# Kernel tuning notes

Measured on AMD Instinct MI355X. Metric: run time of the kernel, lower is better.

## Reference

```python
import jax, jax.numpy as jnp
import numpy as np

N_X, N_U, N_Y = 256, 32, 32
BATCH, T = 16, 8192
LAM_MIN, LAM_MAX = 0.9, 0.995
B_SCALE, D_SCALE = 0.25, 0.25


def setup_inputs() -> dict:
    key = jax.random.key(0)
    k = jax.random.split(key, 6)
    # Orthogonal Q via QR of a random Gaussian matrix (as in the torch module)
    M = jax.random.normal(k[0], (N_X, N_X), dtype=jnp.float32)
    Q, _ = jnp.linalg.qr(M)
    lam = LAM_MIN + (LAM_MAX - LAM_MIN) * jax.random.uniform(k[1], (N_X,), dtype=jnp.float32)
    Bmat = B_SCALE * jax.random.normal(k[2], (N_X, N_U), dtype=jnp.float32)
    # C picks out the first n_y coordinates (C[i, i] = 1)
    C = jnp.eye(N_Y, N_X, dtype=jnp.float32)
    D = D_SCALE * jax.random.normal(k[3], (N_Y, N_U), dtype=jnp.float32)
    x0 = jax.random.normal(k[4], (BATCH, N_X), dtype=jnp.float32)
    u = jax.random.normal(k[5], (BATCH, T, N_U), dtype=jnp.float32)
    return {"x0": x0, "u": u, "Q": Q, "lam": lam, "Bmat": Bmat, "C": C, "D": D}


def _diag_scan(lam, v):
    """Diagonal linear recurrence x_t = lam * x_{t-1} + v_t (x_0 folded into v[:, 0]).

    lam: (N,), v: (B, T, N) -> states x_1..x_T of shape (B, T, N).
    """
    a = jnp.broadcast_to(lam, v.shape)

    def op(l, r):
        a1, b1 = l
        a2, b2 = r
        return a1 * a2, a2 * b1 + b2

    return jax.lax.associative_scan(op, (a, v), axis=1)[1]


def reference(x0, u, Q, lam, Bmat, C, D):
    Bz = Q.T @ Bmat            # (n_x, n_u) modal input matrix
    Cz = C @ Q                 # (n_y, n_x) modal output matrix
    z0 = x0 @ Q                # (B, n_x)   modal initial state
    v = jnp.einsum('btu,nu->btn', u, Bz)   # (B, T, n_x)
    v = v.at[:, 0].add(lam * z0)            # fold lam * z0 into first step
    z_next = _diag_scan(lam, v)             # (B, T, n_x) = z_1..z_T
    # y_t uses z_t for t = 0..T-1 (states[:, :-1] in the original)
    z_prev = jnp.concatenate([z0[:, None, :], z_next[:, :-1]], axis=1)
    y = jnp.einsum('btn,yn->bty', z_prev, Cz) + jnp.einsum('btu,yu->bty', u, D)
    return y
```

## Files before the change

kernel.cpp:

```cpp
#include <hip/hip_runtime.h>

typedef _Float16 half4_t __attribute__((ext_vector_type(4)));
typedef _Float16 half8_t __attribute__((ext_vector_type(8)));
typedef float f32x4 __attribute__((ext_vector_type(4)));

constexpr int NX = 256, NU = 32, NY = 32, BATCH = 16, T = 8192;
constexpr int NC = 64, L = 128;
constexpr int SUBT = 32, NSUB = L / SUBT;
constexpr int KW = NX + NU;
constexpr int VP = 40;
constexpr int ZP = 264;
constexpr int POOLSZ = NX * VP;

__global__ __launch_bounds__(256) void k_pre(
    const float* __restrict__ x0, const float* __restrict__ Q,
    const float* __restrict__ Bm, const float* __restrict__ C,
    const float* __restrict__ D,
    _Float16* __restrict__ Bzh, _Float16* __restrict__ Wh, float* __restrict__ z0)
{
    int o = blockIdx.x * 64 + (threadIdx.x >> 2);
    int p = threadIdx.x & 3;
    if (o >= 20480) {
        if (p == 0) {
            int g = o - 20480, iy = g >> 5, j = g & 31;
            Wh[iy * KW + NX + j] = (_Float16)D[iy * NU + j];
        }
        return;
    }
    float s = 0.f;
    int k0 = p * 64;
    if (o < 8192) {
        int n = o >> 5, j = o & 31;
        for (int k = k0; k < k0 + 64; ++k) s = fmaf(Q[k * NX + n], Bm[k * NU + j], s);
    } else if (o < 16384) {
        int g = o - 8192; int iy = g >> 8, nn = g & 255;
        for (int k = k0; k < k0 + 64; ++k) s = fmaf(C[iy * NX + k], Q[k * NX + nn], s);
    } else {
        int g = o - 16384; int b = g >> 8, nn = g & 255;
        for (int k = k0; k < k0 + 64; ++k) s = fmaf(x0[b * NX + k], Q[k * NX + nn], s);
    }
    s += __shfl_xor(s, 1);
    s += __shfl_xor(s, 2);
    if (p == 0) {
        if (o < 8192) {
            Bzh[o] = (_Float16)s;
        } else if (o < 16384) {
            int g = o - 8192; int iy = g >> 8, nn = g & 255;
            Wh[iy * KW + nn] = (_Float16)s;
        } else {
            z0[o - 16384] = s;
        }
    }
}

__global__ __launch_bounds__(256) void k_phase1(
    const float* __restrict__ u, const float* __restrict__ lam,
    const _Float16* __restrict__ Bzh, float* __restrict__ S)
{
    __shared__ __align__(16) _Float16 ut[2][SUBT][32];

    const int b = blockIdx.x >> 6, c = blockIdx.x & 63, tid = threadIdx.x;
    const int w = tid >> 6, lane = tid & 63, m16 = lane & 15, quad = lane >> 4;

    half8_t bfrag[4];
    #pragma unroll
    for (int i = 0; i < 4; ++i)
        bfrag[i] = *(const half8_t*)&Bzh[((4 * w + i) * 16 + m16) * NU + quad * 8];

    float wr[4][4], wt16[4], l32[4], acc[4];
    #pragma unroll
    for (int i = 0; i < 4; ++i) {
        float la = lam[(4 * w + i) * 16 + m16];
        float p2 = la * la, p4 = p2 * p2, p8 = p4 * p4, p16 = p8 * p8;
        float inv1 = 1.0f / la;
        float inv4 = (inv1 * inv1) * (inv1 * inv1);
        float pq = 1.0f;
        if (quad & 1) pq *= inv4;
        if (quad & 2) pq *= inv4 * inv4;
        float w0 = (p16 * p8 * p4 * p2 * la) * pq;
        wr[i][0] = w0;
        wr[i][1] = w0 * inv1;
        wr[i][2] = wr[i][1] * inv1;
        wr[i][3] = wr[i][2] * inv1;
        wt16[i] = 1.0f / p16;
        l32[i] = p16 * p16;
        acc[i] = 0.f;
    }

    const float* ug = u + ((size_t)(b * T) + (size_t)c * L) * NU;

    for (int sub = 0; sub < NSUB; ++sub) {
        {
            float4 uu = *(const float4*)(ug + (size_t)sub * SUBT * NU + tid * 4);
            int tr = tid >> 3, cb = ((tid & 7) * 4 + (tr & 3) * 8) & 31;
            half4_t h; h.x = (_Float16)uu.x; h.y = (_Float16)uu.y;
            h.z = (_Float16)uu.z; h.w = (_Float16)uu.w;
            *(half4_t*)&ut[sub & 1][tr][cb] = h;
        }
        __syncthreads();
        int rot = (m16 & 3) * 8;
        half8_t af0 = *(const half8_t*)&ut[sub & 1][m16][(quad * 8 + rot) & 31];
        half8_t af1 = *(const half8_t*)&ut[sub & 1][16 + m16][(quad * 8 + rot) & 31];
        #pragma unroll
        for (int i = 0; i < 4; ++i) {
            f32x4 z4 = {0.f, 0.f, 0.f, 0.f};
            f32x4 v0 = __builtin_amdgcn_mfma_f32_16x16x32_f16(af0, bfrag[i], z4, 0, 0, 0);
            f32x4 v1 = __builtin_amdgcn_mfma_f32_16x16x32_f16(af1, bfrag[i], z4, 0, 0, 0);
            float s0 = wr[i][0] * v0[0] + wr[i][1] * v0[1] + wr[i][2] * v0[2] + wr[i][3] * v0[3];
            float s1 = wr[i][0] * v1[0] + wr[i][1] * v1[1] + wr[i][2] * v1[2] + wr[i][3] * v1[3];
            acc[i] = fmaf(l32[i], acc[i], fmaf(wt16[i], s1, s0));
        }
    }
    #pragma unroll
    for (int i = 0; i < 4; ++i) {
        acc[i] += __shfl_xor(acc[i], 16);
        acc[i] += __shfl_xor(acc[i], 32);
    }
    float out = quad == 0 ? acc[0] : quad == 1 ? acc[1] : quad == 2 ? acc[2] : acc[3];
    S[(size_t)blockIdx.x * NX + (4 * w + quad) * 16 + m16] = out;
}

__global__ __launch_bounds__(256) void k_phase2(
    const float* __restrict__ z0, const float* __restrict__ lam,
    const float* __restrict__ S, float* __restrict__ P)
{
    int b = blockIdx.x, n = threadIdx.x;
    float ln = lam[n], lamL = ln;
    #pragma unroll
    for (int i = 0; i < 7; ++i) lamL *= lamL;
    float cur = z0[b * NX + n];
    P[(size_t)(b * NC) * NX + n] = cur;
    for (int c = 1; c < NC; ++c) {
        cur = fmaf(lamL, cur, S[(size_t)(b * NC + c - 1) * NX + n]);
        P[(size_t)(b * NC + c) * NX + n] = cur;
    }
}

__global__ __launch_bounds__(256) void k_phase3(
    const float* __restrict__ u, const float* __restrict__ lam,
    const _Float16* __restrict__ Bzh, const _Float16* __restrict__ Wh,
    const float* __restrict__ P, float* __restrict__ y)
{
    __shared__ __align__(16) _Float16 ut[2][SUBT][32];
    __shared__ __align__(16) _Float16 pool[POOLSZ];

    const int b = blockIdx.x >> 6, c = blockIdx.x & 63, tid = threadIdx.x;
    const int w = tid >> 6, lane = tid & 63, m16 = lane & 15, quad = lane >> 4;
    const int tw = w & 1, yw = w >> 1;

    half8_t bfrag[4];
    #pragma unroll
    for (int i = 0; i < 4; ++i)
        bfrag[i] = *(const half8_t*)&Bzh[((4 * w + i) * 16 + m16) * NU + quad * 8];
    half8_t wfrag[9];
    #pragma unroll
    for (int kk = 0; kk < 9; ++kk)
        wfrag[kk] = *(const half8_t*)&Wh[(yw * 16 + m16) * KW + kk * 32 + quad * 8];
    half8_t triA[2];
    #pragma unroll
    for (int tt = 0; tt < 2; ++tt) {
        #pragma unroll
        for (int j = 0; j < 8; ++j)
            triA[tt][j] = (_Float16)((quad * 8 + j < tt * 16 + m16) ? 1.f : 0.f);
    }

    float lamn[4], inv1[4], iq[4], i16p[4], fq[4], f16p[4], l32[4], p[4];
    #pragma unroll
    for (int i = 0; i < 4; ++i) {
        int ni = (4 * w + i) * 16 + m16;
        float la = lam[ni];
        lamn[i] = la;
        float p2 = la * la, p4 = p2 * p2, p8 = p4 * p4, p16 = p8 * p8;
        float iv = 1.0f / la;
        inv1[i] = iv;
        float iv4 = (iv * iv) * (iv * iv);
        float pqi = 1.0f, pqf = 1.0f;
        if (quad & 1) { pqi *= iv4; pqf *= p4; }
        if (quad & 2) { pqi *= iv4 * iv4; pqf *= p8; }
        iq[i] = iv * pqi;
        fq[i] = pqf;
        i16p[i] = 1.0f / p16;
        f16p[i] = p16;
        l32[i] = p16 * p16;
        p[i] = P[(size_t)(b * NC + c) * NX + ni];
    }

    const float* ug = u + ((size_t)(b * T) + (size_t)c * L) * NU;
    float* yg = y + ((size_t)(b * T) + (size_t)c * L) * NY;

    for (int sub = 0; sub < NSUB; ++sub) {
        {
            float4 uu = *(const float4*)(ug + (size_t)sub * SUBT * NU + tid * 4);
            int tr = tid >> 3, cb = ((tid & 7) * 4 + (tr & 3) * 8) & 31;
            half4_t h; h.x = (_Float16)uu.x; h.y = (_Float16)uu.y;
            h.z = (_Float16)uu.z; h.w = (_Float16)uu.w;
            *(half4_t*)&ut[sub & 1][tr][cb] = h;
        }
        __syncthreads();

        int rot = (m16 & 3) * 8;
        half8_t af0 = *(const half8_t*)&ut[sub & 1][m16][(quad * 8 + rot) & 31];
        half8_t af1 = *(const half8_t*)&ut[sub & 1][16 + m16][(quad * 8 + rot) & 31];
        float partial[4];
        #pragma unroll
        for (int i = 0; i < 4; ++i) {
            int ni = (4 * w + i) * 16 + m16;
            f32x4 z4 = {0.f, 0.f, 0.f, 0.f};
            f32x4 v0 = __builtin_amdgcn_mfma_f32_16x16x32_f16(af0, bfrag[i], z4, 0, 0, 0);
            f32x4 v1 = __builtin_amdgcn_mfma_f32_16x16x32_f16(af1, bfrag[i], z4, 0, 0, 0);
            float ps = 0.f;
            float sc = iq[i];
            half4_t h0, h1;
            #pragma unroll
            for (int r = 0; r < 4; ++r) {
                float a0 = v0[r] * sc;
                float a1 = v1[r] * (sc * i16p[i]);
                ps += a0 + a1;
                h0[r] = (_Float16)a0;
                h1[r] = (_Float16)a1;
                sc *= inv1[i];
            }
            partial[i] = ps;
            *(half4_t*)&pool[ni * VP + quad * 4] = h0;
            *(half4_t*)&pool[ni * VP + 16 + quad * 4] = h1;
        }
        __syncthreads();

        f32x4 zp0[4], zp1[4];
        #pragma unroll
        for (int i = 0; i < 4; ++i) {
            int ni = (4 * w + i) * 16 + m16;
            half8_t bV = *(const half8_t*)&pool[ni * VP + quad * 8];
            f32x4 z4 = {0.f, 0.f, 0.f, 0.f};
            zp0[i] = __builtin_amdgcn_mfma_f32_16x16x32_f16(triA[0], bV, z4, 0, 0, 0);
            zp1[i] = __builtin_amdgcn_mfma_f32_16x16x32_f16(triA[1], bV, z4, 0, 0, 0);
        }
        __syncthreads();

        #pragma unroll
        for (int i = 0; i < 4; ++i) {
            int ni = (4 * w + i) * 16 + m16;
            float f = fq[i];
            #pragma unroll
            for (int r = 0; r < 4; ++r) {
                float zv0 = f * (p[i] + zp0[i][r]);
                float zv1 = (f * f16p[i]) * (p[i] + zp1[i][r]);
                pool[(quad * 4 + r) * ZP + ni] = (_Float16)zv0;
                pool[(16 + quad * 4 + r) * ZP + ni] = (_Float16)zv1;
                f *= lamn[i];
            }
        }
        #pragma unroll
        for (int i = 0; i < 4; ++i) {
            float ps = partial[i];
            ps += __shfl_xor(ps, 16);
            ps += __shfl_xor(ps, 32);
            p[i] = l32[i] * (p[i] + ps);
        }
        __syncthreads();

        f32x4 acc = {0.f, 0.f, 0.f, 0.f};
        #pragma unroll
        for (int kk = 0; kk < 8; ++kk) {
            half8_t az = *(const half8_t*)&pool[(tw * 16 + m16) * ZP + kk * 32 + quad * 8];
            acc = __builtin_amdgcn_mfma_f32_16x16x32_f16(az, wfrag[kk], acc, 0, 0, 0);
        }
        {
            half8_t au = *(const half8_t*)&ut[sub & 1][tw * 16 + m16][(quad * 8 + rot) & 31];
            acc = __builtin_amdgcn_mfma_f32_16x16x32_f16(au, wfrag[8], acc, 0, 0, 0);
        }
        #pragma unroll
        for (int r = 0; r < 4; ++r)
            yg[(size_t)(sub * SUBT + tw * 16 + quad * 4 + r) * NY + yw * 16 + m16] = acc[r];
    }
}

extern "C" void kernel_launch(void* const* d_in, const int* in_sizes, int n_in,
                              void* d_out, int out_size, void* d_ws, size_t ws_size,
                              hipStream_t stream) {
    (void)in_sizes; (void)n_in; (void)out_size; (void)ws_size;
    const float* x0  = (const float*)d_in[0];
    const float* u   = (const float*)d_in[1];
    const float* Q   = (const float*)d_in[2];
    const float* lam = (const float*)d_in[3];
    const float* Bm  = (const float*)d_in[4];
    const float* C   = (const float*)d_in[5];
    const float* D   = (const float*)d_in[6];
    float* y = (float*)d_out;

    char* ws = (char*)d_ws;
    _Float16* Bzh = (_Float16*)(ws);
    _Float16* Wh  = (_Float16*)(ws + 16384);
    float*    z0  = (float*)(ws + 34816);
    float*    S   = (float*)(ws + 51200);
    float*    P   = (float*)(ws + 51200 + 1048576);

    k_pre   <<<336, 256, 0, stream>>>(x0, Q, Bm, C, D, Bzh, Wh, z0);
    k_phase1<<<BATCH * NC, 256, 0, stream>>>(u, lam, Bzh, S);
    k_phase2<<<BATCH, 256, 0, stream>>>(z0, lam, S, P);
    k_phase3<<<BATCH * NC, 256, 0, stream>>>(u, lam, Bzh, Wh, P, y);
}
```

Baseline: 119.8 us.

## Fold chunk-prefix carry computation into phase3, removing the phase2 kernel

Drops the serial per-batch phase2 kernel that scanned chunk summaries into carry-in states. Each phase3 block now recomputes its own carry-in by summing all earlier chunk summaries, weighted by powers of lam^L, plus the decayed z0, and stages the result in shared memory. This removes one kernel launch and a long serial 64-step dependency chain that ran on only 16 blocks. In exchange, the carry work becomes redundant and quadratic in chunk count, up to 63 loads per thread in late chunks, and a block-wide barrier is added.

```diff
diff --git a/kernel.cpp b/kernel.cpp
--- a/kernel.cpp
+++ b/kernel.cpp
@@ -120,33 +120,32 @@
     S[(size_t)blockIdx.x * NX + (4 * w + quad) * 16 + m16] = out;
 }
 
-__global__ __launch_bounds__(256) void k_phase2(
-    const float* __restrict__ z0, const float* __restrict__ lam,
-    const float* __restrict__ S, float* __restrict__ P)
-{
-    int b = blockIdx.x, n = threadIdx.x;
-    float ln = lam[n], lamL = ln;
-    #pragma unroll
-    for (int i = 0; i < 7; ++i) lamL *= lamL;
-    float cur = z0[b * NX + n];
-    P[(size_t)(b * NC) * NX + n] = cur;
-    for (int c = 1; c < NC; ++c) {
-        cur = fmaf(lamL, cur, S[(size_t)(b * NC + c - 1) * NX + n]);
-        P[(size_t)(b * NC + c) * NX + n] = cur;
-    }
-}
-
 __global__ __launch_bounds__(256) void k_phase3(
     const float* __restrict__ u, const float* __restrict__ lam,
     const _Float16* __restrict__ Bzh, const _Float16* __restrict__ Wh,
-    const float* __restrict__ P, float* __restrict__ y)
+    const float* __restrict__ S, const float* __restrict__ z0,
+    float* __restrict__ y)
 {
     __shared__ __align__(16) _Float16 ut[2][SUBT][32];
     __shared__ __align__(16) _Float16 pool[POOLSZ];
+    __shared__ float pvec[NX];
 
     const int b = blockIdx.x >> 6, c = blockIdx.x & 63, tid = threadIdx.x;
     const int w = tid >> 6, lane = tid & 63, m16 = lane & 15, quad = lane >> 4;
     const int tw = w & 1, yw = w >> 1;
+
+    {
+        float la = lam[tid], lamL = la;
+        #pragma unroll
+        for (int i = 0; i < 7; ++i) lamL *= lamL;
+        const float* Sb = S + (size_t)(b * NC) * NX;
+        float pv = 0.f, wgt = 1.f;
+        for (int cc = c - 1; cc >= 0; --cc) {
+            pv = fmaf(wgt, Sb[(size_t)cc * NX + tid], pv);
+            wgt *= lamL;
+        }
+        pvec[tid] = fmaf(wgt, z0[b * NX + tid], pv);
+    }
 
     half8_t bfrag[4];
     #pragma unroll
@@ -182,11 +181,15 @@
         i16p[i] = 1.0f / p16;
         f16p[i] = p16;
         l32[i] = p16 * p16;
-        p[i] = P[(size_t)(b * NC + c) * NX + ni];
-    }
+    }
+    __syncthreads();
+    #pragma unroll
+    for (int i = 0; i < 4; ++i)
+        p[i] = pvec[(4 * w + i) * 16 + m16];
 
     const float* ug = u + ((size_t)(b * T) + (size_t)c * L) * NU;
     float* yg = y + ((size_t)(b * T) + (size_t)c * L) * NY;
+    const int rot = (m16 & 3) * 8;
 
     for (int sub = 0; sub < NSUB; ++sub) {
         {
@@ -198,7 +201,6 @@
         }
         __syncthreads();
 
-        int rot = (m16 & 3) * 8;
         half8_t af0 = *(const half8_t*)&ut[sub & 1][m16][(quad * 8 + rot) & 31];
         half8_t af1 = *(const half8_t*)&ut[sub & 1][16 + m16][(quad * 8 + rot) & 31];
         float partial[4];
@@ -293,10 +295,8 @@
     _Float16* Wh  = (_Float16*)(ws + 16384);
     float*    z0  = (float*)(ws + 34816);
     float*    S   = (float*)(ws + 51200);
-    float*    P   = (float*)(ws + 51200 + 1048576);
 
     k_pre   <<<336, 256, 0, stream>>>(x0, Q, Bm, C, D, Bzh, Wh, z0);
     k_phase1<<<BATCH * NC, 256, 0, stream>>>(u, lam, Bzh, S);
-    k_phase2<<<BATCH, 256, 0, stream>>>(z0, lam, S, P);
-    k_phase3<<<BATCH * NC, 256, 0, stream>>>(u, lam, Bzh, Wh, P, y);
+    k_phase3<<<BATCH * NC, 256, 0, stream>>>(u, lam, Bzh, Wh, S, z0, y);
 }
```

Measured after the change: 129.9 us. 1.08x slower.
